# Performance work log

Measured on AMD Instinct MI355X. Metric: run time of the kernel, lower is better.

The kernel has to match this reference:

```python
import jax, jax.numpy as jnp
import numpy as np

B, S, D, H = 4, 1024, 1024, 16
HD = D // H
NEG = 10000.0


def setup_inputs() -> dict:
    key = jax.random.key(0)
    k1, k2, k3 = jax.random.split(key, 3)
    std = 0.02
    return {
        "x": jax.random.normal(k1, (B, S, D), dtype=jnp.float32),
        "mask": jnp.zeros((B, 1, 1, S), dtype=jnp.float32),
        "w_attn": jax.random.normal(k2, (D, 3 * D), dtype=jnp.float32) * std,
        "b_attn": jnp.zeros((1, 3 * D), dtype=jnp.float32),
        "w_proj": jax.random.normal(k3, (D, D), dtype=jnp.float32) * std,
        "b_proj": jnp.zeros((1, D), dtype=jnp.float32),
    }


def reference(x, mask, w_attn, b_attn, w_proj, b_proj):
    b, s, d = x.shape
    # fused QKV projection (Conv1D == dense over last dim)
    qkv = x @ w_attn + b_attn  # [B,S,3D]
    q, k, v = jnp.split(qkv, 3, axis=2)

    def split_heads(t):  # [B,S,D] -> [B,H,S,HD]
        return t.reshape(b, s, H, HD).transpose(0, 2, 1, 3)

    q, k, v = split_heads(q), split_heads(k), split_heads(v)

    w = jnp.einsum("bhqd,bhkd->bhqk", q, k) / jnp.sqrt(jnp.float32(HD))
    # causal mask (lower triangle from lower-right corner)
    i = jnp.arange(s)[:, None]
    j = jnp.arange(s)[None, :]
    bmask = (i >= j).astype(w.dtype)[None, None]  # [1,1,S,S]
    w = w * bmask - NEG * (1.0 - bmask)
    w = w + mask
    w = jax.nn.softmax(w, axis=-1)  # attn_dropout is identity at inference
    a = jnp.einsum("bhqk,bhkd->bhqd", w, v)
    a = a.transpose(0, 2, 1, 3).reshape(b, s, d)  # merge heads
    a = a @ w_proj + b_proj  # resid_dropout identity at inference
    return (a, w)
```

## Files before the change

### kernel.cpp

```cpp
#include <hip/hip_runtime.h>
#include <hip/hip_bf16.h>

constexpr int Bb = 4, Ss = 1024, Dd = 1024, Hh = 16;

typedef __attribute__((ext_vector_type(8))) short short8;
typedef __attribute__((ext_vector_type(4))) float f32x4;

static __device__ __forceinline__ ushort f2bf(float f) {
  union { __hip_bfloat16 h; ushort u; } cv;
  cv.h = __float2bfloat16(f);
  return cv.u;
}

static __device__ __forceinline__ void gl_lds16(const ushort* g, ushort* l) {
  __builtin_amdgcn_global_load_lds(
      (const __attribute__((address_space(1))) void*)g,
      (__attribute__((address_space(3))) void*)l, 16, 0, 0);
}

__global__ __launch_bounds__(256) void cast_f32_bf16(
    const float* __restrict__ in, ushort* __restrict__ out) {
  const int i = (blockIdx.x * 256 + threadIdx.x) * 4;
  const float4 v = *(const float4*)&in[i];
  ushort4 o;
  o.x = f2bf(v.x); o.y = f2bf(v.y); o.z = f2bf(v.z); o.w = f2bf(v.w);
  *(ushort4*)&out[i] = o;
}

__global__ __launch_bounds__(256) void transpose_cast(
    const float* __restrict__ in, ushort* __restrict__ out, int R, int C) {
  __shared__ float T[32][33];
  const int c0 = blockIdx.x * 32, r0 = blockIdx.y * 32;
  const int t = threadIdx.x;
  const int r = t >> 3, c4 = (t & 7) * 4;
  const float4 v = *(const float4*)&in[(size_t)(r0 + r) * C + c0 + c4];
  T[r][c4 + 0] = v.x; T[r][c4 + 1] = v.y;
  T[r][c4 + 2] = v.z; T[r][c4 + 3] = v.w;
  __syncthreads();
  const int cc = t >> 3, rr4 = (t & 7) * 4;
  ushort4 o;
  o.x = f2bf(T[rr4 + 0][cc]); o.y = f2bf(T[rr4 + 1][cc]);
  o.z = f2bf(T[rr4 + 2][cc]); o.w = f2bf(T[rr4 + 3][cc]);
  *(ushort4*)&out[(size_t)(c0 + cc) * R + r0 + rr4] = o;
}

template <int BM, int BN, bool OUT_BF16, bool V_SPLIT>
__global__ __launch_bounds__(256) void gemm_bt(
    const ushort* __restrict__ A, const ushort* __restrict__ Bt,
    const float* __restrict__ bias, void* __restrict__ Cout,
    ushort* __restrict__ vt, int M, int N, int K) {
  constexpr int TM = BM / 32, TN = BN / 32;
  __shared__ ushort As[2][BM * 32];
  __shared__ ushort Bs[2][BN * 32];
  const int tid = threadIdx.x;
  const int wv = tid >> 6, lane = tid & 63;
  const int l15 = lane & 15, quad = lane >> 4;
  const int ln4 = lane >> 2, kp = (lane & 3) * 8;
  const int m0 = blockIdx.y * BM, n0 = blockIdx.x * BN;
  const int wrow = (wv >> 1) * (BM / 2), wcol = (wv & 1) * (BN / 2);

  const ushort* Arow = &A[(size_t)(m0 + wv * 16 + ln4) * K + kp];
  const ushort* Brow = &Bt[(size_t)(n0 + wv * 16 + ln4) * K + kp];

  f32x4 acc[TM][TN] = {};

#pragma unroll
  for (int u = 0; u < BM / 64; u++)
    gl_lds16(Arow + (size_t)u * 64 * K, &As[0][wv * 512 + u * 2048]);
#pragma unroll
  for (int u = 0; u < BN / 64; u++)
    gl_lds16(Brow + (size_t)u * 64 * K, &Bs[0][wv * 512 + u * 2048]);
  __syncthreads();

  const int nt = K / 32;
  int cur = 0;
  for (int t = 0; t < nt; ++t) {
    if (t + 1 < nt) {
      const int k1 = (t + 1) * 32;
#pragma unroll
      for (int u = 0; u < BM / 64; u++)
        gl_lds16(Arow + (size_t)u * 64 * K + k1,
                 &As[cur ^ 1][wv * 512 + u * 2048]);
#pragma unroll
      for (int u = 0; u < BN / 64; u++)
        gl_lds16(Brow + (size_t)u * 64 * K + k1,
                 &Bs[cur ^ 1][wv * 512 + u * 2048]);
    }
    short8 af[TM], bfr[TN];
#pragma unroll
    for (int i = 0; i < TM; i++)
      af[i] = *(const short8*)&As[cur][(wrow + i * 16 + l15) * 32 + quad * 8];
#pragma unroll
    for (int j = 0; j < TN; j++)
      bfr[j] = *(const short8*)&Bs[cur][(wcol + j * 16 + l15) * 32 + quad * 8];
#pragma unroll
    for (int i = 0; i < TM; i++)
#pragma unroll
      for (int j = 0; j < TN; j++)
        acc[i][j] = __builtin_amdgcn_mfma_f32_16x16x32_bf16(af[i], bfr[j],
                                                            acc[i][j], 0, 0, 0);
    __syncthreads();
    cur ^= 1;
  }

  if (V_SPLIT && n0 >= 2048) {
#pragma unroll
    for (int j = 0; j < TN; j++) {
      const int col = n0 + wcol + j * 16 + l15;
      const int cv = col - 2048;
      const int hh = cv >> 6, dd = cv & 63;
      const float bv = bias[col];
#pragma unroll
      for (int i = 0; i < TM; i++) {
        const int row0 = m0 + wrow + i * 16 + quad * 4;
        const int bidx = row0 >> 10, jt = row0 & 1023;
        ushort4 o;
        o.x = f2bf(acc[i][j][0] + bv);
        o.y = f2bf(acc[i][j][1] + bv);
        o.z = f2bf(acc[i][j][2] + bv);
        o.w = f2bf(acc[i][j][3] + bv);
        *(ushort4*)&vt[((size_t)((bidx << 4) + hh) * 64 + dd) * 1024 + jt] = o;
      }
    }
  } else {
#pragma unroll
    for (int j = 0; j < TN; j++) {
      const int col = n0 + wcol + j * 16 + l15;
      const float bv = bias[col];
#pragma unroll
      for (int i = 0; i < TM; i++) {
#pragma unroll
        for (int r = 0; r < 4; r++) {
          const int row = m0 + wrow + i * 16 + quad * 4 + r;
          const float v = acc[i][j][r] + bv;
          if (OUT_BF16)
            ((ushort*)Cout)[(size_t)row * N + col] = f2bf(v);
          else
            ((float*)Cout)[(size_t)row * N + col] = v;
        }
      }
    }
  }
}

__global__ __launch_bounds__(256) void attn_mfma(
    const ushort* __restrict__ qkvb,
    const ushort* __restrict__ vt,
    const float* __restrict__ mask,
    float* __restrict__ w_out,
    ushort* __restrict__ ab) {
  constexpr int LDP = 1032;
  __shared__ ushort Ps[16 * LDP];
  __shared__ float PM[16][4];
  __shared__ float PSum[16][4];

  const int f = blockIdx.y * 64 + blockIdx.x;
  const int swz = (f & 7) * 512 + (f >> 3);
  const int qt = swz & 63, bh = swz >> 6;

  const int b = bh >> 4, h = bh & 15;
  const int q0 = qt * 16;
  const int tid = threadIdx.x;
  const int wv = tid >> 6, lane = tid & 63;
  const int l15 = lane & 15, quad = lane >> 4;

  const size_t rowQ = (size_t)((b << 10) + q0 + l15) * 3072 + h * 64;
  const short8 qf0 = *(const short8*)&qkvb[rowQ + quad * 8];
  const short8 qf1 = *(const short8*)&qkvb[rowQ + 32 + quad * 8];

  float sreg[16][4];

#pragma unroll
  for (int i = 0; i < 16; i++) {
    const int j0 = (wv + 4 * i) * 16;
    const int col = j0 + l15;
    const float mv = mask[(b << 10) + col];
    if (j0 <= q0 + 15) {
      const size_t rowK = (size_t)((b << 10) + j0 + l15) * 3072 + 1024 + h * 64;
      const short8 kf0 = *(const short8*)&qkvb[rowK + quad * 8];
      const short8 kf1 = *(const short8*)&qkvb[rowK + 32 + quad * 8];
      f32x4 c = {0.f, 0.f, 0.f, 0.f};
      c = __builtin_amdgcn_mfma_f32_16x16x32_bf16(qf0, kf0, c, 0, 0, 0);
      c = __builtin_amdgcn_mfma_f32_16x16x32_bf16(qf1, kf1, c, 0, 0, 0);
#pragma unroll
      for (int r = 0; r < 4; r++)
        sreg[i][r] =
            (col <= q0 + quad * 4 + r ? c[r] * 0.125f : -10000.0f) + mv;
    } else {
#pragma unroll
      for (int r = 0; r < 4; r++) sreg[i][r] = -10000.0f + mv;
    }
  }

#pragma unroll
  for (int r = 0; r < 4; r++) {
    float m = sreg[0][r];
#pragma unroll
    for (int i = 1; i < 16; i++) m = fmaxf(m, sreg[i][r]);
#pragma unroll
    for (int off = 1; off < 16; off <<= 1) m = fmaxf(m, __shfl_xor(m, off));
    if (l15 == 0) PM[quad * 4 + r][wv] = m;
  }
  __syncthreads();

  float mrow[4];
#pragma unroll
  for (int r = 0; r < 4; r++) {
    const f32x4 pm4 = *(const f32x4*)&PM[quad * 4 + r][0];
    mrow[r] = fmaxf(fmaxf(pm4[0], pm4[1]), fmaxf(pm4[2], pm4[3]));
  }

  float psum[4] = {0.f, 0.f, 0.f, 0.f};
#pragma unroll
  for (int i = 0; i < 16; i++)
#pragma unroll
    for (int r = 0; r < 4; r++) {
      const float e = __expf(fminf(sreg[i][r] - mrow[r], 0.0f));
      sreg[i][r] = e;
      psum[r] += e;
    }
#pragma unroll
  for (int r = 0; r < 4; r++) {
    float s = psum[r];
#pragma unroll
    for (int off = 1; off < 16; off <<= 1) s += __shfl_xor(s, off);
    if (l15 == 0) PSum[quad * 4 + r][wv] = s;
  }
  __syncthreads();

  float inv4[4];
#pragma unroll
  for (int r = 0; r < 4; r++) {
    const f32x4 ps4 = *(const f32x4*)&PSum[quad * 4 + r][0];
    inv4[r] = 1.0f / fmaxf(ps4[0] + ps4[1] + ps4[2] + ps4[3], 1e-30f);
  }

#pragma unroll
  for (int i = 0; i < 16; i++) {
    const int j0 = (wv + 4 * i) * 16;
#pragma unroll
    for (int r = 0; r < 4; r++) {
      const float p = sreg[i][r] * inv4[r];
      w_out[((size_t)(bh << 10) + q0 + quad * 4 + r) * 1024 + j0 + l15] = p;
      Ps[(quad * 4 + r) * LDP + j0 + l15] = f2bf(p);
    }
  }
  __syncthreads();

  f32x4 oacc = {0.f, 0.f, 0.f, 0.f};
  const int nch = (q0 + 16 + 31) >> 5;
  const ushort* vbase = vt + ((size_t)bh * 64 + wv * 16 + l15) * 1024;
  for (int c = 0; c < nch; c++) {
    const int k0 = c * 32;
    const short8 pf = *(const short8*)&Ps[l15 * LDP + k0 + quad * 8];
    const short8 vf = *(const short8*)&vbase[k0 + quad * 8];
    oacc = __builtin_amdgcn_mfma_f32_16x16x32_bf16(pf, vf, oacc, 0, 0, 0);
  }
#pragma unroll
  for (int r = 0; r < 4; r++) {
    ab[(size_t)((b << 10) + q0 + quad * 4 + r) * 1024 + h * 64 + wv * 16 +
       l15] = f2bf(oacc[r]);
  }
}

extern "C" void kernel_launch(void* const* d_in, const int* in_sizes, int n_in,
                              void* d_out, int out_size, void* d_ws,
                              size_t ws_size, hipStream_t stream) {
  const float* x = (const float*)d_in[0];
  const float* mask = (const float*)d_in[1];
  const float* w_attn = (const float*)d_in[2];
  const float* b_attn = (const float*)d_in[3];
  const float* w_proj = (const float*)d_in[4];
  const float* b_proj = (const float*)d_in[5];

  float* out_a = (float*)d_out;
  float* out_w = out_a + (size_t)Bb * Ss * Dd;

  char* ws = (char*)d_ws;
  ushort* xb   = (ushort*)(ws);
  ushort* wta  = (ushort*)(ws + (8u << 20));
  ushort* wtp  = (ushort*)(ws + (14u << 20));
  ushort* qkvb = (ushort*)(ws + (16u << 20));
  ushort* vt   = (ushort*)(ws + (40u << 20));
  ushort* ab   = (ushort*)(ws + (48u << 20));

  cast_f32_bf16<<<(Bb * Ss * Dd) / 1024, 256, 0, stream>>>(x, xb);
  transpose_cast<<<dim3(3 * Dd / 32, Dd / 32), 256, 0, stream>>>(w_attn, wta,
                                                                 Dd, 3 * Dd);
  transpose_cast<<<dim3(Dd / 32, Dd / 32), 256, 0, stream>>>(w_proj, wtp, Dd,
                                                             Dd);
  gemm_bt<128, 128, true, true><<<dim3(3 * Dd / 128, Bb * Ss / 128), 256, 0,
                                  stream>>>(xb, wta, b_attn, qkvb, vt,
                                            Bb * Ss, 3 * Dd, Dd);
  attn_mfma<<<dim3(Ss / 16, Bb * Hh), 256, 0, stream>>>(qkvb, vt, mask, out_w,
                                                        ab);
  gemm_bt<128, 64, false, false><<<dim3(Dd / 64, Bb * Ss / 128), 256, 0,
                                   stream>>>(ab, wtp, b_proj, out_a, nullptr,
                                             Bb * Ss, Dd, Dd);
}
```

Before: 443.7 us.

## Triple-buffer GEMM LDS loads with explicit vmcnt waits; batch V loads in PV loop

```diff
diff --git a/kernel.cpp b/kernel.cpp
--- a/kernel.cpp
+++ b/kernel.cpp
@@ -50,8 +50,9 @@
     const float* __restrict__ bias, void* __restrict__ Cout,
     ushort* __restrict__ vt, int M, int N, int K) {
   constexpr int TM = BM / 32, TN = BN / 32;
-  __shared__ ushort As[2][BM * 32];
-  __shared__ ushort Bs[2][BN * 32];
+  constexpr int NLD = BM / 64 + BN / 64;
+  __shared__ ushort As[3][BM * 32];
+  __shared__ ushort Bs[3][BN * 32];
   const int tid = threadIdx.x;
   const int wv = tid >> 6, lane = tid & 63;
   const int l15 = lane & 15, quad = lane >> 4;
@@ -64,28 +65,31 @@
 
   f32x4 acc[TM][TN] = {};
 
-#pragma unroll
-  for (int u = 0; u < BM / 64; u++)
-    gl_lds16(Arow + (size_t)u * 64 * K, &As[0][wv * 512 + u * 2048]);
-#pragma unroll
-  for (int u = 0; u < BN / 64; u++)
-    gl_lds16(Brow + (size_t)u * 64 * K, &Bs[0][wv * 512 + u * 2048]);
-  __syncthreads();
-
   const int nt = K / 32;
-  int cur = 0;
+
+#define STAGE_T(tt, buf)                                                     \
+  {                                                                          \
+    const int kk = (tt) * 32;                                                \
+    _Pragma("unroll") for (int u = 0; u < BM / 64; u++)                      \
+        gl_lds16(Arow + (size_t)u * 64 * K + kk,                             \
+                 &As[buf][wv * 512 + u * 2048]);                             \
+    _Pragma("unroll") for (int u = 0; u < BN / 64; u++)                      \
+        gl_lds16(Brow + (size_t)u * 64 * K + kk,                             \
+                 &Bs[buf][wv * 512 + u * 2048]);                             \
+  }
+
+  STAGE_T(0, 0);
+  STAGE_T(1, 1);
+
   for (int t = 0; t < nt; ++t) {
-    if (t + 1 < nt) {
-      const int k1 = (t + 1) * 32;
-#pragma unroll
-      for (int u = 0; u < BM / 64; u++)
-        gl_lds16(Arow + (size_t)u * 64 * K + k1,
-                 &As[cur ^ 1][wv * 512 + u * 2048]);
-#pragma unroll
-      for (int u = 0; u < BN / 64; u++)
-        gl_lds16(Brow + (size_t)u * 64 * K + k1,
-                 &Bs[cur ^ 1][wv * 512 + u * 2048]);
-    }
+    const int cur = t % 3;
+    if (t + 1 < nt)
+      asm volatile("s_waitcnt vmcnt(%0)" ::"n"(NLD) : "memory");
+    else
+      asm volatile("s_waitcnt vmcnt(0)" ::: "memory");
+    __builtin_amdgcn_s_barrier();
+    __builtin_amdgcn_sched_barrier(0);
+
     short8 af[TM], bfr[TN];
 #pragma unroll
     for (int i = 0; i < TM; i++)
@@ -93,15 +97,19 @@
 #pragma unroll
     for (int j = 0; j < TN; j++)
       bfr[j] = *(const short8*)&Bs[cur][(wcol + j * 16 + l15) * 32 + quad * 8];
+
+    if (t + 2 < nt) STAGE_T(t + 2, (t + 2) % 3);
+
 #pragma unroll
     for (int i = 0; i < TM; i++)
 #pragma unroll
       for (int j = 0; j < TN; j++)
         acc[i][j] = __builtin_amdgcn_mfma_f32_16x16x32_bf16(af[i], bfr[j],
                                                             acc[i][j], 0, 0, 0);
-    __syncthreads();
-    cur ^= 1;
-  }
+    __builtin_amdgcn_sched_barrier(0);
+    __builtin_amdgcn_s_barrier();
+  }
+#undef STAGE_T
 
   if (V_SPLIT && n0 >= 2048) {
 #pragma unroll
@@ -250,11 +258,20 @@
   f32x4 oacc = {0.f, 0.f, 0.f, 0.f};
   const int nch = (q0 + 16 + 31) >> 5;
   const ushort* vbase = vt + ((size_t)bh * 64 + wv * 16 + l15) * 1024;
-  for (int c = 0; c < nch; c++) {
-    const int k0 = c * 32;
-    const short8 pf = *(const short8*)&Ps[l15 * LDP + k0 + quad * 8];
-    const short8 vf = *(const short8*)&vbase[k0 + quad * 8];
-    oacc = __builtin_amdgcn_mfma_f32_16x16x32_bf16(pf, vf, oacc, 0, 0, 0);
+  for (int c0 = 0; c0 < nch; c0 += 4) {
+    short8 vbuf[4];
+#pragma unroll
+    for (int u = 0; u < 4; u++)
+      if (c0 + u < nch)
+        vbuf[u] = *(const short8*)&vbase[(c0 + u) * 32 + quad * 8];
+#pragma unroll
+    for (int u = 0; u < 4; u++)
+      if (c0 + u < nch) {
+        const short8 pf =
+            *(const short8*)&Ps[l15 * LDP + (c0 + u) * 32 + quad * 8];
+        oacc = __builtin_amdgcn_mfma_f32_16x16x32_bf16(pf, vbuf[u], oacc,
+                                                       0, 0, 0);
+      }
   }
 #pragma unroll
   for (int r = 0; r < 4; r++) {
```

After: 430.2 us, median of 2. 3.0% less time.
